# Optimization experiments

Hardware: AMD Instinct MI355X
Metric: run time of the kernel (lower is better)

Reference implementation:

```python
import jax, jax.numpy as jnp
import numpy as np

L = 5        # num_layers
DIM = 128    # data dim
SPLIT = DIM // 2   # 64
H = 64       # hidden_dim (fixed in AffineCouplingLayer)
OUT = DIM - SPLIT  # 64
B = 262144   # batch


def setup_inputs() -> dict:
    key = jax.random.key(0)
    ks = jax.random.split(key, 13)

    def p(k, shape, fan_in):
        return jax.random.normal(k, shape, jnp.float32) * (1.0 / np.sqrt(fan_in))

    inp = {
        "x": jax.random.normal(ks[0], (B, DIM), jnp.float32),
        # s_net params, stacked over layers. Linear stored as [in, out] (y = x @ W + b)
        "s_W1": p(ks[1], (L, SPLIT, H), SPLIT), "s_b1": jnp.zeros((L, H), jnp.float32),
        "s_W2": p(ks[2], (L, H, H), H),         "s_b2": jnp.zeros((L, H), jnp.float32),
        "s_W3": p(ks[3], (L, H, OUT), H),       "s_b3": jnp.zeros((L, OUT), jnp.float32),
        # t_net params
        "t_W1": p(ks[4], (L, SPLIT, H), SPLIT), "t_b1": jnp.zeros((L, H), jnp.float32),
        "t_W2": p(ks[5], (L, H, H), H),         "t_b2": jnp.zeros((L, H), jnp.float32),
        "t_W3": p(ks[6], (L, H, OUT), H),       "t_b3": jnp.zeros((L, OUT), jnp.float32),
    }
    return inp


def _mlp(x0, W1, b1, W2, b2, W3, b3):
    # 3-layer MLP with LeakyReLU(0.01) between layers (torch default slope)
    h = jax.nn.leaky_relu(x0 @ W1 + b1, 0.01)
    h = jax.nn.leaky_relu(h @ W2 + b2, 0.01)
    return h @ W3 + b3


def reference(x, s_W1, s_b1, s_W2, s_b2, s_W3, s_b3,
              t_W1, t_b1, t_W2, t_b2, t_W3, t_b3):
    x0 = x[:, :SPLIT]          # never changes across layers (matches source)
    x1 = x[:, SPLIT:]
    log_det = jnp.zeros(x.shape[0], x.dtype)
    for l in range(L):
        s = jnp.tanh(_mlp(x0, s_W1[l], s_b1[l], s_W2[l], s_b2[l], s_W3[l], s_b3[l]))
        t = _mlp(x0, t_W1[l], t_b1[l], t_W2[l], t_b2[l], t_W3[l], t_b3[l])
        x1 = x1 * jnp.exp(s) + t
        log_det = log_det + jnp.sum(s, axis=1)
    z = jnp.concatenate([x0, x1], axis=1)
    return z, log_det
```

## Files before the change

kernel.cpp:

```cpp
#include <hip/hip_runtime.h>

typedef __fp16 f16;
typedef __fp16 f16x2 __attribute__((ext_vector_type(2)));
typedef __fp16 f16x8 __attribute__((ext_vector_type(8)));
typedef float f32x4 __attribute__((ext_vector_type(4)));
typedef float f32x16 __attribute__((ext_vector_type(16)));

__device__ __forceinline__ unsigned pkrtz(float a, float b) {
    f16x2 r = __builtin_amdgcn_cvt_pkrtz(a, b);
    return __builtin_bit_cast(unsigned, r);
}

__device__ __forceinline__ f16x8 pack4(unsigned a, unsigned b, unsigned c, unsigned d) {
    union { unsigned u[4]; f16x8 v; } r;
    r.u[0] = a; r.u[1] = b; r.u[2] = c; r.u[3] = d;
    return r.v;
}

__global__ __launch_bounds__(512) void pack_w(
    const float* __restrict__ sW1, const float* __restrict__ sW2, const float* __restrict__ sW3,
    const float* __restrict__ tW1, const float* __restrict__ tW2, const float* __restrict__ tW3,
    f16* __restrict__ wp) {
    int mat = blockIdx.x;
    int layer = mat / 6;
    int rem = mat % 6;
    int fi = threadIdx.x >> 6;
    int lane = threadIdx.x & 63;
    int tile = fi >> 2, kt = fi & 3;
    int h = lane >> 5;
    int m = (lane & 31) + 32 * tile;
    const float* Wt[6] = {sW1, sW2, sW3, tW1, tW2, tW3};
    const float* W = Wt[rem] + layer * 4096;
    f16x8 v;
#pragma unroll
    for (int e = 0; e < 8; ++e) {
        int k = 16 * kt + 4 * h + (e & 3) + ((e >> 2) << 3);
        v[e] = (f16)W[k * 64 + m];
    }
    *(f16x8*)(wp + ((size_t)mat * 8 + fi) * 512 + lane * 8) = v;
}

__global__ __launch_bounds__(512) void pack_b(
    const float* __restrict__ sb1, const float* __restrict__ sb2, const float* __restrict__ sb3,
    const float* __restrict__ tb1, const float* __restrict__ tb2, const float* __restrict__ tb3,
    float* __restrict__ wb) {
    int i = blockIdx.x * 512 + threadIdx.x;
    if (i >= 1920) return;
    int l = i / 384, r = i % 384, mat = r / 64, j = r % 64;
    const float* B[6] = {sb1, sb2, sb3, tb1, tb2, tb3};
    wb[l * 384 + mat * 64 + j] = B[mat][l * 64 + j];
}

__device__ __forceinline__ void bias_init(const float* bias, int h, f32x16 c[2]) {
#pragma unroll
    for (int t = 0; t < 2; ++t) {
#pragma unroll
        for (int r4 = 0; r4 < 4; ++r4) {
            f32x4 bb = *(const f32x4*)(bias + 32 * t + 8 * r4 + 4 * h);
            c[t][4 * r4 + 0] = bb[0];
            c[t][4 * r4 + 1] = bb[1];
            c[t][4 * r4 + 2] = bb[2];
            c[t][4 * r4 + 3] = bb[3];
        }
    }
}

__device__ __forceinline__ void gemm_pair(const f16* wS, const f16* wT,
                                          const f16x8 inS[4], const f16x8 inT[4],
                                          const float* bS, const float* bT,
                                          int lane, f32x16 cs[2], f32x16 ct[2]) {
    const int h = (lane >> 5) & 1;
    bias_init(bS, h, cs);
    bias_init(bT, h, ct);
#pragma unroll
    for (int t = 0; t < 2; ++t) {
#pragma unroll
        for (int kt = 0; kt < 4; ++kt) {
            f16x8 a = *(const f16x8*)(wS + (t * 4 + kt) * 512 + lane * 8);
            f16x8 b = *(const f16x8*)(wT + (t * 4 + kt) * 512 + lane * 8);
            cs[t] = __builtin_amdgcn_mfma_f32_32x32x16_f16(a, inS[kt], cs[t], 0, 0, 0);
            ct[t] = __builtin_amdgcn_mfma_f32_32x32x16_f16(b, inT[kt], ct[t], 0, 0, 0);
        }
    }
}

__device__ __forceinline__ void relu_pack(const f32x16 c[2], f16x8 o[4]) {
    const f16 hc = (f16)0.01f;
    const f16x8 c001 = {hc, hc, hc, hc, hc, hc, hc, hc};
#pragma unroll
    for (int kt = 0; kt < 4; ++kt) {
        const int tl = kt >> 1;
        const int base = 8 * (kt & 1);
        f16x8 v = pack4(pkrtz(c[tl][base + 0], c[tl][base + 1]),
                        pkrtz(c[tl][base + 2], c[tl][base + 3]),
                        pkrtz(c[tl][base + 4], c[tl][base + 5]),
                        pkrtz(c[tl][base + 6], c[tl][base + 7]));
        o[kt] = __builtin_elementwise_max(v, v * c001);
    }
}

#define BUFSZ 25344

__global__ __launch_bounds__(512, 2)
void flow_main(const float* __restrict__ x, const f16* __restrict__ wp,
               float* __restrict__ out, int nrows) {
    __shared__ f16 wl[2 * BUFSZ];
    const int tid = threadIdx.x;
    const int lane = tid & 63;
    const int wv = tid >> 6;
    const int h = lane >> 5;
    const int n = (blockIdx.x * 8 + wv) * 32 + (lane & 31);
    const float* xr = x + (size_t)n * 128;
    float* zr = out + (size_t)n * 128;
    const float* wbias_g = (const float*)((const char*)wp + 491520);

    f32x4 stg[6];
    f32x4 stgb = {0.f, 0.f, 0.f, 0.f};
    {
        const f32x4* src = (const f32x4*)wp;
#pragma unroll
        for (int i = 0; i < 6; ++i) stg[i] = src[tid + 512 * i];
        if (tid < 96) stgb = ((const f32x4*)wbias_g)[tid];
    }

    f16x8 x0f[4];
#pragma unroll
    for (int kt = 0; kt < 4; ++kt) {
        f32x4 a = *(const f32x4*)(xr + 16 * kt + 4 * h);
        f32x4 b = *(const f32x4*)(xr + 16 * kt + 8 + 4 * h);
        *(f32x4*)(zr + 16 * kt + 4 * h) = a;
        *(f32x4*)(zr + 16 * kt + 8 + 4 * h) = b;
        x0f[kt] = pack4(pkrtz(a[0], a[1]), pkrtz(a[2], a[3]), pkrtz(b[0], b[1]), pkrtz(b[2], b[3]));
    }

    f32x4 x1v[8];
#pragma unroll
    for (int t = 0; t < 2; ++t)
#pragma unroll
        for (int r4 = 0; r4 < 4; ++r4)
            x1v[t * 4 + r4] = *(const f32x4*)(xr + 64 + 32 * t + 8 * r4 + 4 * h);

    {
        f32x4* dst = (f32x4*)wl;
#pragma unroll
        for (int i = 0; i < 6; ++i) dst[tid + 512 * i] = stg[i];
        if (tid < 96) ((f32x4*)((char*)wl + 49152))[tid] = stgb;
    }
    __syncthreads();

    float ld = 0.f;
#pragma unroll 1
    for (int l = 0; l < 5; ++l) {
        const int cur = l & 1;
        const f16* bufc = wl + cur * BUFSZ;
        const float* bias = (const float*)(bufc + 24576);

        if (l < 4) {
            const f32x4* src = (const f32x4*)(wp + (size_t)(l + 1) * 24576);
#pragma unroll
            for (int i = 0; i < 6; ++i) stg[i] = src[tid + 512 * i];
            if (tid < 96) stgb = ((const f32x4*)(wbias_g + (l + 1) * 384))[tid];
        }

        f32x16 cs[2], ct[2];
        gemm_pair(bufc, bufc + 12288, x0f, x0f, bias + 0, bias + 192, lane, cs, ct);
        f16x8 h1s[4], h1t[4];
        relu_pack(cs, h1s);
        relu_pack(ct, h1t);
        f32x16 c2s[2], c2t[2];
        gemm_pair(bufc + 4096, bufc + 16384, h1s, h1t, bias + 64, bias + 256, lane, c2s, c2t);
        f16x8 h2s[4], h2t[4];
        relu_pack(c2s, h2s);
        relu_pack(c2t, h2t);

        if (l < 4) {
            f32x4* dst = (f32x4*)(wl + (cur ^ 1) * BUFSZ);
#pragma unroll
            for (int i = 0; i < 6; ++i) dst[tid + 512 * i] = stg[i];
            if (tid < 96) ((f32x4*)((char*)(wl + (cur ^ 1) * BUFSZ) + 49152))[tid] = stgb;
        }

        f32x16 c3s[2], c3t[2];
        gemm_pair(bufc + 8192, bufc + 20480, h2s, h2t, bias + 128, bias + 320, lane, c3s, c3t);

#pragma unroll
        for (int t = 0; t < 2; ++t) {
#pragma unroll
            for (int r = 0; r < 16; ++r) {
                float u = __builtin_amdgcn_exp2f(2.8853900817779268f * c3s[t][r]);
                float rc = __builtin_amdgcn_rcpf(u + 1.f);
                float s = fmaf(-2.f, rc, 1.f);
                ld += s;
                float e = __builtin_amdgcn_exp2f(fmaf(-2.8853900817779268f, rc, 1.4426950408889634f));
                x1v[t * 4 + (r >> 2)][r & 3] =
                    fmaf(x1v[t * 4 + (r >> 2)][r & 3], e, c3t[t][r]);
            }
        }

        __syncthreads();
    }

#pragma unroll
    for (int t = 0; t < 2; ++t)
#pragma unroll
        for (int r4 = 0; r4 < 4; ++r4)
            *(f32x4*)(zr + 64 + 32 * t + 8 * r4 + 4 * h) = x1v[t * 4 + r4];

    float tot = ld + __shfl_xor(ld, 32);
    if (h == 0) out[(size_t)nrows * 128 + n] = tot;
}

extern "C" void kernel_launch(void* const* d_in, const int* in_sizes, int n_in,
                              void* d_out, int out_size, void* d_ws, size_t ws_size,
                              hipStream_t stream) {
    const float* x   = (const float*)d_in[0];
    const float* sW1 = (const float*)d_in[1];
    const float* sb1 = (const float*)d_in[2];
    const float* sW2 = (const float*)d_in[3];
    const float* sb2 = (const float*)d_in[4];
    const float* sW3 = (const float*)d_in[5];
    const float* sb3 = (const float*)d_in[6];
    const float* tW1 = (const float*)d_in[7];
    const float* tb1 = (const float*)d_in[8];
    const float* tW2 = (const float*)d_in[9];
    const float* tb2 = (const float*)d_in[10];
    const float* tW3 = (const float*)d_in[11];
    const float* tb3 = (const float*)d_in[12];

    f16* wp = (f16*)d_ws;
    float* wb = (float*)((char*)d_ws + 491520);
    int nrows = in_sizes[0] / 128;

    pack_w<<<30, 512, 0, stream>>>(sW1, sW2, sW3, tW1, tW2, tW3, wp);
    pack_b<<<4, 512, 0, stream>>>(sb1, sb2, sb3, tb1, tb2, tb3, wb);
    flow_main<<<nrows / 256, 512, 0, stream>>>(x, wp, (float*)d_out, nrows);
}
```

Baseline: 129.3 us.

## Split waves into paired and sequential MLP schedules and raise MFMA priority

Half the waves in each block (wv>=4) now run the s-network and t-network MLPs one after another rather than interleaved. They apply the tanh/exp transcendental epilogue for s before computing t. s_setprio brackets are also added around the MFMA loops. The goal is to stagger MFMA and transcendental phases across waves so the matrix and vector units overlap better. The cost is code-path divergence between waves, higher instruction footprint, and shorter MFMA dependency chains in the sequential path.

```diff
diff --git a/kernel.cpp b/kernel.cpp
--- a/kernel.cpp
+++ b/kernel.cpp
@@ -72,6 +72,7 @@
     const int h = (lane >> 5) & 1;
     bias_init(bS, h, cs);
     bias_init(bT, h, ct);
+    __builtin_amdgcn_s_setprio(1);
 #pragma unroll
     for (int t = 0; t < 2; ++t) {
 #pragma unroll
@@ -82,6 +83,23 @@
             ct[t] = __builtin_amdgcn_mfma_f32_32x32x16_f16(b, inT[kt], ct[t], 0, 0, 0);
         }
     }
+    __builtin_amdgcn_s_setprio(0);
+}
+
+__device__ __forceinline__ void gemm1(const f16* w, const f16x8 in[4],
+                                      const float* bias, int lane, f32x16 c[2]) {
+    const int h = (lane >> 5) & 1;
+    bias_init(bias, h, c);
+    __builtin_amdgcn_s_setprio(1);
+#pragma unroll
+    for (int mt = 0; mt < 2; ++mt) {
+#pragma unroll
+        for (int kt = 0; kt < 4; ++kt) {
+            f16x8 wf = *(const f16x8*)(w + (mt * 4 + kt) * 512 + lane * 8);
+            c[mt] = __builtin_amdgcn_mfma_f32_32x32x16_f16(wf, in[kt], c[mt], 0, 0, 0);
+        }
+    }
+    __builtin_amdgcn_s_setprio(0);
 }
 
 __device__ __forceinline__ void relu_pack(const f32x16 c[2], f16x8 o[4]) {
@@ -97,6 +115,19 @@
                         pkrtz(c[tl][base + 6], c[tl][base + 7]));
         o[kt] = __builtin_elementwise_max(v, v * c001);
     }
+}
+
+__device__ __forceinline__ void mlp3_1(const f16* w, const f16x8 x0f[4],
+                                       const float* bias, int lane, f32x16 out[2]) {
+    f32x16 c1[2];
+    gemm1(w, x0f, bias, lane, c1);
+    f16x8 h1[4];
+    relu_pack(c1, h1);
+    f32x16 c2[2];
+    gemm1(w + 4096, h1, bias + 64, lane, c2);
+    f16x8 h2[4];
+    relu_pack(c2, h2);
+    gemm1(w + 8192, h2, bias + 128, lane, out);
 }
 
 #define BUFSZ 25344
@@ -113,6 +144,7 @@
     const float* xr = x + (size_t)n * 128;
     float* zr = out + (size_t)n * 128;
     const float* wbias_g = (const float*)((const char*)wp + 491520);
+    const bool depair = (wv & 4);
 
     f32x4 stg[6];
     f32x4 stgb = {0.f, 0.f, 0.f, 0.f};
@@ -162,38 +194,73 @@
             if (tid < 96) stgb = ((const f32x4*)(wbias_g + (l + 1) * 384))[tid];
         }
 
-        f32x16 cs[2], ct[2];
-        gemm_pair(bufc, bufc + 12288, x0f, x0f, bias + 0, bias + 192, lane, cs, ct);
-        f16x8 h1s[4], h1t[4];
-        relu_pack(cs, h1s);
-        relu_pack(ct, h1t);
-        f32x16 c2s[2], c2t[2];
-        gemm_pair(bufc + 4096, bufc + 16384, h1s, h1t, bias + 64, bias + 256, lane, c2s, c2t);
-        f16x8 h2s[4], h2t[4];
-        relu_pack(c2s, h2s);
-        relu_pack(c2t, h2t);
-
-        if (l < 4) {
-            f32x4* dst = (f32x4*)(wl + (cur ^ 1) * BUFSZ);
-#pragma unroll
-            for (int i = 0; i < 6; ++i) dst[tid + 512 * i] = stg[i];
-            if (tid < 96) ((f32x4*)((char*)(wl + (cur ^ 1) * BUFSZ) + 49152))[tid] = stgb;
-        }
-
         f32x16 c3s[2], c3t[2];
-        gemm_pair(bufc + 8192, bufc + 20480, h2s, h2t, bias + 128, bias + 320, lane, c3s, c3t);
-
-#pragma unroll
-        for (int t = 0; t < 2; ++t) {
-#pragma unroll
-            for (int r = 0; r < 16; ++r) {
-                float u = __builtin_amdgcn_exp2f(2.8853900817779268f * c3s[t][r]);
-                float rc = __builtin_amdgcn_rcpf(u + 1.f);
-                float s = fmaf(-2.f, rc, 1.f);
-                ld += s;
-                float e = __builtin_amdgcn_exp2f(fmaf(-2.8853900817779268f, rc, 1.4426950408889634f));
-                x1v[t * 4 + (r >> 2)][r & 3] =
-                    fmaf(x1v[t * 4 + (r >> 2)][r & 3], e, c3t[t][r]);
+
+        if (!depair) {
+            f32x16 cs[2], ct[2];
+            gemm_pair(bufc, bufc + 12288, x0f, x0f, bias + 0, bias + 192, lane, cs, ct);
+            f16x8 h1s[4], h1t[4];
+            relu_pack(cs, h1s);
+            relu_pack(ct, h1t);
+            f32x16 c2s[2], c2t[2];
+            gemm_pair(bufc + 4096, bufc + 16384, h1s, h1t, bias + 64, bias + 256, lane, c2s, c2t);
+            f16x8 h2s[4], h2t[4];
+            relu_pack(c2s, h2s);
+            relu_pack(c2t, h2t);
+
+            if (l < 4) {
+                f32x4* dst = (f32x4*)(wl + (cur ^ 1) * BUFSZ);
+#pragma unroll
+                for (int i = 0; i < 6; ++i) dst[tid + 512 * i] = stg[i];
+                if (tid < 96) ((f32x4*)((char*)(wl + (cur ^ 1) * BUFSZ) + 49152))[tid] = stgb;
+            }
+
+            gemm_pair(bufc + 8192, bufc + 20480, h2s, h2t, bias + 128, bias + 320, lane, c3s, c3t);
+        } else {
+            mlp3_1(bufc, x0f, bias + 0, lane, c3s);
+
+            if (l < 4) {
+                f32x4* dst = (f32x4*)(wl + (cur ^ 1) * BUFSZ);
+#pragma unroll
+                for (int i = 0; i < 6; ++i) dst[tid + 512 * i] = stg[i];
+                if (tid < 96) ((f32x4*)((char*)(wl + (cur ^ 1) * BUFSZ) + 49152))[tid] = stgb;
+            }
+
+#pragma unroll
+            for (int t = 0; t < 2; ++t) {
+#pragma unroll
+                for (int r = 0; r < 16; ++r) {
+                    float u = __builtin_amdgcn_exp2f(2.8853900817779268f * c3s[t][r]);
+                    float rc = __builtin_amdgcn_rcpf(u + 1.f);
+                    float s = fmaf(-2.f, rc, 1.f);
+                    ld += s;
+                    float e = __builtin_amdgcn_exp2f(fmaf(-2.8853900817779268f, rc, 1.4426950408889634f));
+                    x1v[t * 4 + (r >> 2)][r & 3] *= e;
+                }
+            }
+
+            mlp3_1(bufc + 12288, x0f, bias + 192, lane, c3t);
+
+#pragma unroll
+            for (int t = 0; t < 2; ++t)
+#pragma unroll
+                for (int r = 0; r < 16; ++r)
+                    x1v[t * 4 + (r >> 2)][r & 3] += c3t[t][r];
+        }
+
+        if (!depair) {
+#pragma unroll
+            for (int t = 0; t < 2; ++t) {
+#pragma unroll
+                for (int r = 0; r < 16; ++r) {
+                    float u = __builtin_amdgcn_exp2f(2.8853900817779268f * c3s[t][r]);
+                    float rc = __builtin_amdgcn_rcpf(u + 1.f);
+                    float s = fmaf(-2.f, rc, 1.f);
+                    ld += s;
+                    float e = __builtin_amdgcn_exp2f(fmaf(-2.8853900817779268f, rc, 1.4426950408889634f));
+                    x1v[t * 4 + (r >> 2)][r & 3] =
+                        fmaf(x1v[t * 4 + (r >> 2)][r & 3], e, c3t[t][r]);
+                }
             }
         }
 
```

Measured after the change: 140.0 us. 8.3% more time.
